# Optimization experiments

Measured on AMD Instinct MI355X. Metric: run time of the kernel, lower is better.

The kernel has to match this reference:

```python
import jax, jax.numpy as jnp
import numpy as np

B, C, H, W = 32, 256, 56, 56
NH, WS, SS = 8, 7, 3
N = WS * WS
EPS = 1e-5


def _rel_pos_index(ws):
    ch, cw = np.meshgrid(np.arange(ws), np.arange(ws), indexing='ij')
    coords = np.stack([ch.reshape(-1), cw.reshape(-1)])  # (2, N)
    rel = coords[:, :, None] - coords[:, None, :]        # (2, N, N)
    rel = rel.transpose(1, 2, 0)
    rel[:, :, 0] += ws - 1
    rel[:, :, 1] += ws - 1
    rel[:, :, 0] *= 2 * ws - 1
    return rel.sum(-1)  # (N, N) int


def _attn_mask(Hh, Ww, ws, ss):
    img = np.zeros((Hh, Ww), dtype=np.float32)
    cnt = 0
    for hs in (slice(0, -ws), slice(-ws, -ss), slice(-ss, None)):
        for wsl in (slice(0, -ws), slice(-ws, -ss), slice(-ss, None)):
            img[hs, wsl] = cnt
            cnt += 1
    mw = img.reshape(Hh // ws, ws, Ww // ws, ws).transpose(0, 2, 1, 3).reshape(-1, ws * ws)
    am = mw[:, None, :] - mw[:, :, None]
    return np.where(am != 0, np.float32(-100.0), np.float32(0.0))  # (nW, N, N)

RPI = _rel_pos_index(WS)
AMASK = _attn_mask(H, W, WS, SS)


def _ln(x, w, b):
    mu = x.mean(-1, keepdims=True)
    var = ((x - mu) ** 2).mean(-1, keepdims=True)
    return (x - mu) * jax.lax.rsqrt(var + EPS) * w + b


def setup_inputs() -> dict:
    key = jax.random.key(0)
    ks = jax.random.split(key, 10)
    s = 0.02
    return {
        'x': jax.random.normal(ks[0], (B, C, H, W), jnp.float32),
        'qkv_w': jax.random.normal(ks[1], (3 * C, C), jnp.float32) * s,
        'q_bias': jnp.zeros((C,), jnp.float32),
        'v_bias': jnp.zeros((C,), jnp.float32),
        'proj_w': jax.random.normal(ks[2], (C, C), jnp.float32) * s,
        'proj_b': jnp.zeros((C,), jnp.float32),
        'rpb_table': jax.random.normal(ks[3], ((2 * WS - 1) * (2 * WS - 1), NH), jnp.float32) * s,
        'norm1_w': jnp.ones((C,), jnp.float32),
        'norm1_b': jnp.zeros((C,), jnp.float32),
        'norm2_w': jnp.ones((C,), jnp.float32),
        'norm2_b': jnp.zeros((C,), jnp.float32),
        'fc1_w': jax.random.normal(ks[4], (4 * C, C), jnp.float32) * s,
        'fc1_b': jnp.zeros((4 * C,), jnp.float32),
        'fc2_w': jax.random.normal(ks[5], (C, 4 * C), jnp.float32) * s,
        'fc2_b': jnp.zeros((C,), jnp.float32),
    }


def reference(x, qkv_w, q_bias, v_bias, proj_w, proj_b, rpb_table,
              norm1_w, norm1_b, norm2_w, norm2_b, fc1_w, fc1_b, fc2_w, fc2_b):
    b = x.shape[0]
    hd = C // NH
    scale = hd ** -0.5
    nWh, nWw = H // WS, W // WS
    nW = nWh * nWw

    # (B,C,H,W) -> (B, L, C)
    xs = x.transpose(0, 2, 3, 1).reshape(b, H * W, C)
    shortcut = xs
    xn = _ln(xs, norm1_w, norm1_b).reshape(b, H, W, C)
    # cyclic shift
    xn = jnp.roll(xn, (-SS, -SS), axis=(1, 2))
    # window partition -> (B*nW, N, C)
    xw = xn.reshape(b, nWh, WS, nWw, WS, C).transpose(0, 1, 3, 2, 4, 5).reshape(b * nW, N, C)

    qkv_bias = jnp.concatenate([q_bias, jnp.zeros_like(v_bias), v_bias])
    qkv = xw @ qkv_w.T + qkv_bias                      # (B_, N, 3C)
    qkv = qkv.reshape(b * nW, N, 3, NH, hd).transpose(2, 0, 3, 1, 4)
    q, k, v = qkv[0], qkv[1], qkv[2]                   # (B_, NH, N, hd)

    attn = jnp.einsum('whnd,whmd->whnm', q * scale, k)  # (B_, NH, N, N)
    bias = rpb_table[RPI.reshape(-1)].reshape(N, N, NH).transpose(2, 0, 1)
    attn = attn + bias[None]
    attn = attn.reshape(b, nW, NH, N, N) + jnp.asarray(AMASK)[None, :, None]
    attn = jax.nn.softmax(attn.reshape(b * nW, NH, N, N), axis=-1)

    out = jnp.einsum('whnm,whmd->whnd', attn, v)        # (B_, NH, N, hd)
    out = out.transpose(0, 2, 1, 3).reshape(b * nW, N, C)
    out = out @ proj_w.T + proj_b

    # window reverse + un-shift
    out = out.reshape(b, nWh, nWw, WS, WS, C).transpose(0, 1, 3, 2, 4, 5).reshape(b, H, W, C)
    out = jnp.roll(out, (SS, SS), axis=(1, 2)).reshape(b, H * W, C)

    xs = shortcut + out
    h = _ln(xs, norm2_w, norm2_b)
    h = jax.nn.relu(h @ fc1_w.T + fc1_b) @ fc2_w.T + fc2_b
    xs = xs + h
    return xs.reshape(b, H, W, C).transpose(0, 3, 1, 2)
```

## Files before the change

kernel.cpp:

```cpp
#include <hip/hip_runtime.h>
#include <math.h>

#define EPS 1e-5f

constexpr int Bc = 32, Cc = 256, Hc = 56, Wc = 56;
constexpr int NHc = 8, HDc = 32, WSc = 7, SSc = 3;
constexpr int NTOK = 49;
constexpr int NWIN = 64;
constexpr int Lc = Hc * Wc;
constexpr int Mrows = Bc * NWIN * NTOK;
constexpr int GIMG = 8;
constexpr int NGRP = Bc / GIMG;
constexpr int ROWS_G = GIMG * Lc;
constexpr int WIN_G = GIMG * NWIN;

typedef short bf16x8 __attribute__((ext_vector_type(8)));
typedef float f32x4 __attribute__((ext_vector_type(4)));
typedef unsigned short u16x8 __attribute__((ext_vector_type(8)));

__device__ __forceinline__ float bf2f(unsigned short u) {
    return __uint_as_float(((unsigned)u) << 16);
}
__device__ __forceinline__ unsigned short f2bf(float f) {
    unsigned x = __float_as_uint(f);
    return (unsigned short)((x + 0x7fffu + ((x >> 16) & 1u)) >> 16);
}

__global__ __launch_bounds__(256) void k_prep(const float* __restrict__ qkv_w,
                                              const float* __restrict__ proj_w,
                                              const float* __restrict__ w1,
                                              const float* __restrict__ w2,
                                              const float* __restrict__ qb,
                                              const float* __restrict__ vb,
                                              unsigned short* __restrict__ qkv_wb,
                                              unsigned short* __restrict__ proj_wb,
                                              unsigned short* __restrict__ w1t,
                                              unsigned short* __restrict__ w2t,
                                              float* __restrict__ qkvb) {
    int i = blockIdx.x * 256 + threadIdx.x;
    if (i < 768) qkvb[i] = (i < 256) ? qb[i] : ((i < 512) ? 0.f : vb[i - 512]);
    if (i < 196608) qkv_wb[i] = f2bf(qkv_w[i]);
    if (i < 65536)  proj_wb[i] = f2bf(proj_w[i]);
    if (i < 262144) {
        int n1 = i >> 8, k1 = i & 255;
        w1t[((n1 >> 4) * 32 + (k1 >> 3)) * 128 + (n1 & 15) * 8 + (k1 & 7)] = f2bf(w1[i]);
        int n2 = i >> 10, k2 = i & 1023;
        w2t[((k2 >> 6) * 32 + (n2 >> 4) * 2 + ((k2 >> 5) & 1)) * 512 +
            ((k2 >> 3) & 3) * 128 + (n2 & 15) * 8 + (k2 & 7)] = f2bf(w2[i]);
    }
}

__global__ __launch_bounds__(256) void k_ln1_part(const float* __restrict__ x,
                                                  const float* __restrict__ n1w,
                                                  const float* __restrict__ n1b,
                                                  unsigned short* __restrict__ xw,
                                                  unsigned short* __restrict__ xres,
                                                  int b0) {
    __shared__ float s[Cc * 57];
    __shared__ float mu[Wc], rs[Wc];
    int bg = blockIdx.x / Hc, h = blockIdx.x % Hc;
    int b = b0 + bg;
    int t = threadIdx.x;
    const float* xp = x + ((size_t)b * Cc) * Lc + h * Wc;
    for (int idx = t; idx < Cc * Wc; idx += 256) {
        int c = idx / Wc, w = idx % Wc;
        s[c * 57 + w] = xp[(size_t)c * Lc + w];
    }
    __syncthreads();
    int lane = t & 63, wv = t >> 6;
    for (int p = wv; p < Wc; p += 4) {
        float sum = 0.f, sq = 0.f;
        #pragma unroll
        for (int k = 0; k < 4; ++k) {
            float v = s[(lane + 64 * k) * 57 + p];
            sum += v; sq += v * v;
        }
        #pragma unroll
        for (int off = 32; off; off >>= 1) {
            sum += __shfl_xor(sum, off);
            sq  += __shfl_xor(sq, off);
        }
        if (lane == 0) {
            float m = sum / Cc;
            mu[p] = m;
            rs[p] = rsqrtf(sq / Cc - m * m + EPS);
        }
    }
    __syncthreads();
    float wc_ = n1w[t], bc_ = n1b[t];
    int hr = (h + Hc - SSc) % Hc;
    int whh = hr / WSc, th = hr % WSc;
    for (int p = 0; p < Wc; ++p) {
        float raw = s[t * 57 + p];
        xres[((size_t)bg * Lc + h * Wc + p) * Cc + t] = f2bf(raw);
        int wr = (p + Wc - SSc) % Wc;
        int www = wr / WSc, tw = wr % WSc;
        int row = (b * NWIN + whh * 8 + www) * NTOK + th * WSc + tw;
        float v = (raw - mu[p]) * rs[p] * wc_ + bc_;
        xw[(size_t)row * Cc + t] = f2bf(v);
    }
}

__global__ __launch_bounds__(256) void k_gemm_mfma(const unsigned short* __restrict__ A,
                                                   const unsigned short* __restrict__ W,
                                                   const float* __restrict__ bias,
                                                   unsigned short* __restrict__ outb,
                                                   int K, int Nd) {
    __shared__ unsigned short As[128 * 32];
    __shared__ unsigned short Bs[128 * 32];
    int t = threadIdx.x;
    int l = t & 63, w = t >> 6;
    int wm = w & 1, wn = w >> 1;
    int m0 = blockIdx.x * 128, n0 = blockIdx.y * 128;
    int lr = l & 15, lg = l >> 4;

    f32x4 acc[4][4];
    #pragma unroll
    for (int i = 0; i < 4; ++i)
        #pragma unroll
        for (int j = 0; j < 4; ++j)
            acc[i][j] = (f32x4){0.f, 0.f, 0.f, 0.f};

    for (int kt = 0; kt < K; kt += 32) {
        #pragma unroll
        for (int s = 0; s < 2; ++s) {
            int cid = t + s * 256;
            int row = cid >> 2, ch = cid & 3;
            u16x8 va = *(const u16x8*)(A + (size_t)(m0 + row) * K + kt + ch * 8);
            u16x8 vb = *(const u16x8*)(W + (size_t)(n0 + row) * K + kt + ch * 8);
            int off = (row * 32 + ch * 8) ^ ((row & 7) << 3);
            *(u16x8*)&As[off] = va;
            *(u16x8*)&Bs[off] = vb;
        }
        __syncthreads();
        bf16x8 af[4], bfr[4];
        #pragma unroll
        for (int i = 0; i < 4; ++i) {
            int ra = wm * 64 + i * 16 + lr;
            af[i] = *(bf16x8*)&As[(ra * 32 + lg * 8) ^ ((ra & 7) << 3)];
            int rb = wn * 64 + i * 16 + lr;
            bfr[i] = *(bf16x8*)&Bs[(rb * 32 + lg * 8) ^ ((rb & 7) << 3)];
        }
        #pragma unroll
        for (int i = 0; i < 4; ++i)
            #pragma unroll
            for (int j = 0; j < 4; ++j)
                acc[i][j] = __builtin_amdgcn_mfma_f32_16x16x32_bf16(af[i], bfr[j], acc[i][j], 0, 0, 0);
        __syncthreads();
    }

    float bj[4];
    #pragma unroll
    for (int j = 0; j < 4; ++j) bj[j] = bias[n0 + wn * 64 + j * 16 + lr];
    #pragma unroll
    for (int i = 0; i < 4; ++i)
        #pragma unroll
        for (int j = 0; j < 4; ++j) {
            int col = n0 + wn * 64 + j * 16 + lr;
            #pragma unroll
            for (int r = 0; r < 4; ++r) {
                int row = m0 + wm * 64 + i * 16 + lg * 4 + r;
                outb[(size_t)row * Nd + col] = f2bf(acc[i][j][r] + bj[j]);
            }
        }
}

__global__ __launch_bounds__(256) void k_gemm_proj(const unsigned short* __restrict__ A,
                                                   const unsigned short* __restrict__ W,
                                                   const float* __restrict__ bias,
                                                   const unsigned short* __restrict__ xres,
                                                   unsigned short* __restrict__ xs) {
    __shared__ unsigned short As[128 * 32];
    __shared__ unsigned short Bs[128 * 32];
    constexpr int K = 256;
    int t = threadIdx.x;
    int l = t & 63, w = t >> 6;
    int wm = w & 1, wn = w >> 1;
    int m0 = blockIdx.x * 128, n0 = blockIdx.y * 128;
    int lr = l & 15, lg = l >> 4;

    f32x4 acc[4][4];
    #pragma unroll
    for (int i = 0; i < 4; ++i)
        #pragma unroll
        for (int j = 0; j < 4; ++j)
            acc[i][j] = (f32x4){0.f, 0.f, 0.f, 0.f};

    for (int kt = 0; kt < K; kt += 32) {
        #pragma unroll
        for (int s = 0; s < 2; ++s) {
            int cid = t + s * 256;
            int row = cid >> 2, ch = cid & 3;
            u16x8 va = *(const u16x8*)(A + (size_t)(m0 + row) * K + kt + ch * 8);
            u16x8 vb = *(const u16x8*)(W + (size_t)(n0 + row) * K + kt + ch * 8);
            int off = (row * 32 + ch * 8) ^ ((row & 7) << 3);
            *(u16x8*)&As[off] = va;
            *(u16x8*)&Bs[off] = vb;
        }
        __syncthreads();
        bf16x8 af[4], bfr[4];
        #pragma unroll
        for (int i = 0; i < 4; ++i) {
            int ra = wm * 64 + i * 16 + lr;
            af[i] = *(bf16x8*)&As[(ra * 32 + lg * 8) ^ ((ra & 7) << 3)];
            int rb = wn * 64 + i * 16 + lr;
            bfr[i] = *(bf16x8*)&Bs[(rb * 32 + lg * 8) ^ ((rb & 7) << 3)];
        }
        #pragma unroll
        for (int i = 0; i < 4; ++i)
            #pragma unroll
            for (int j = 0; j < 4; ++j)
                acc[i][j] = __builtin_amdgcn_mfma_f32_16x16x32_bf16(af[i], bfr[j], acc[i][j], 0, 0, 0);
        __syncthreads();
    }

    float bj[4];
    #pragma unroll
    for (int j = 0; j < 4; ++j) bj[j] = bias[n0 + wn * 64 + j * 16 + lr];
    #pragma unroll
    for (int i = 0; i < 4; ++i)
        #pragma unroll
        for (int j = 0; j < 4; ++j) {
            int col = n0 + wn * 64 + j * 16 + lr;
            #pragma unroll
            for (int r = 0; r < 4; ++r) {
                int row = m0 + wm * 64 + i * 16 + lg * 4 + r;
                int wl = row / NTOK, tok = row - wl * NTOK;
                int bg = wl >> 6, wi = wl & 63;
                int hr = (wi >> 3) * 7 + tok / 7;
                int wr = (wi & 7) * 7 + tok % 7;
                int hh = hr + SSc; if (hh >= Hc) hh -= Hc;
                int ww = wr + SSc; if (ww >= Wc) ww -= Wc;
                size_t didx = ((size_t)bg * Lc + hh * Wc + ww) * Cc + col;
                float res = bf2f(xres[didx]);
                xs[didx] = f2bf(res + acc[i][j][r] + bj[j]);
            }
        }
}

__global__ __launch_bounds__(256) void k_attn(const unsigned short* __restrict__ qkv,
                                              const float* __restrict__ rpb,
                                              unsigned short* __restrict__ outb) {
    __shared__ unsigned short lds[4 * 6144 + 1352];
    unsigned short* rpbs = &lds[4 * 6144];
    int t = threadIdx.x;
    int w = t >> 6, l = t & 63;
    int lr = l & 15, lg = l >> 4;
    unsigned short* wl = &lds[w * 6144];
    unsigned short* Qs = wl;
    unsigned short* Ks = wl + 2048;
    unsigned short* Pm = wl;
    unsigned short* Vt = wl + 4096;

    for (int i = t; i < 1352; i += 256) rpbs[i] = f2bf(rpb[i]);

    int gid = blockIdx.x * 4 + w;
    int b_ = gid >> 3, hh = gid & 7;
    const unsigned short* base = qkv + (size_t)b_ * NTOK * 768 + hh * HDc;

    {
        int j = l;
        u16x8 vq[4], vk[4], vv[4];
        if (j < NTOK) {
            const unsigned short* rp = base + j * 768;
            #pragma unroll
            for (int s = 0; s < 4; ++s) {
                vq[s] = *(const u16x8*)(rp + s * 8);
                vk[s] = *(const u16x8*)(rp + 256 + s * 8);
                vv[s] = *(const u16x8*)(rp + 512 + s * 8);
            }
        } else {
            u16x8 z = {0, 0, 0, 0, 0, 0, 0, 0};
            #pragma unroll
            for (int s = 0; s < 4; ++s) { vq[s] = z; vk[s] = z; vv[s] = z; }
        }
        #pragma unroll
        for (int s = 0; s < 4; ++s) {
            int off = (j * 32 + s * 8) ^ ((j & 7) << 3);
            *(u16x8*)&Qs[off] = vq[s];
            *(u16x8*)&Ks[off] = vk[s];
        }
        #pragma unroll
        for (int s = 0; s < 4; ++s)
            #pragma unroll
            for (int e = 0; e < 8; ++e) {
                int d = s * 8 + e;
                Vt[d * 64 + (j ^ ((d & 7) << 3))] = ((unsigned short*)&vv[s])[e];
            }
    }
    __syncthreads();

    bf16x8 aq[4], bk[4];
    #pragma unroll
    for (int mt = 0; mt < 4; ++mt) {
        int row = mt * 16 + lr;
        int off = (row * 32 + lg * 8) ^ ((row & 7) << 3);
        aq[mt] = *(bf16x8*)&Qs[off];
        bk[mt] = *(bf16x8*)&Ks[off];
    }
    f32x4 sc[4][4];
    #pragma unroll
    for (int mt = 0; mt < 4; ++mt)
        #pragma unroll
        for (int nt = 0; nt < 4; ++nt)
            sc[mt][nt] = __builtin_amdgcn_mfma_f32_16x16x32_bf16(
                aq[mt], bk[nt], (f32x4){0.f, 0.f, 0.f, 0.f}, 0, 0, 0);

    const float scale = 0.17677669529663687f;
    int wi = b_ & 63, wh = wi >> 3, wwc = wi & 7;
    int jh[4], jw[4], ridJ[4];
    #pragma unroll
    for (int nt = 0; nt < 4; ++nt) {
        int j = nt * 16 + lr;
        jh[nt] = j / 7; jw[nt] = j - jh[nt] * 7;
        int gh = wh * 7 + jh[nt], gw = wwc * 7 + jw[nt];
        int rh = gh < 49 ? 0 : (gh < 53 ? 1 : 2);
        int rw = gw < 49 ? 0 : (gw < 53 ? 1 : 2);
        ridJ[nt] = rh * 3 + rw;
    }

    float rowrcp[4][4];
    #pragma unroll
    for (int mt = 0; mt < 4; ++mt) {
        #pragma unroll
        for (int r = 0; r < 4; ++r) {
            int i = mt * 16 + lg * 4 + r;
            int ih = i / 7, iw = i - ih * 7;
            int gh = wh * 7 + ih, gw = wwc * 7 + iw;
            int rhI = gh < 49 ? 0 : (gh < 53 ? 1 : 2);
            int rwI = gw < 49 ? 0 : (gw < 53 ? 1 : 2);
            int ridI = rhI * 3 + rwI;
            bool ivalid = (i < NTOK);
            float vals[4];
            float vmax = -1e30f;
            #pragma unroll
            for (int nt = 0; nt < 4; ++nt) {
                int j = nt * 16 + lr;
                float v = -1e30f;
                if (ivalid && j < NTOK) {
                    int rpi = (ih - jh[nt] + 6) * 13 + (iw - jw[nt] + 6);
                    float bv = bf2f(rpbs[rpi * 8 + hh]);
                    float msk = (ridI == ridJ[nt]) ? 0.f : -100.f;
                    v = sc[mt][nt][r] * scale + bv + msk;
                }
                vals[nt] = v;
                vmax = fmaxf(vmax, v);
            }
            #pragma unroll
            for (int off = 1; off < 16; off <<= 1)
                vmax = fmaxf(vmax, __shfl_xor(vmax, off));
            float s = 0.f;
            unsigned short pb[4];
            #pragma unroll
            for (int nt = 0; nt < 4; ++nt) {
                float e = (vals[nt] > -1e29f) ? __expf(vals[nt] - vmax) : 0.f;
                s += e;
                pb[nt] = f2bf(e);
            }
            #pragma unroll
            for (int off = 1; off < 16; off <<= 1)
                s += __shfl_xor(s, off);
            rowrcp[mt][r] = 1.f / s;
            #pragma unroll
            for (int nt = 0; nt < 4; ++nt) {
                int j = nt * 16 + lr;
                Pm[(i * 64 + j) ^ ((i & 7) << 3)] = pb[nt];
            }
        }
    }

    f32x4 o[4][2];
    #pragma unroll
    for (int mt = 0; mt < 4; ++mt)
        #pragma unroll
        for (int nt = 0; nt < 2; ++nt)
            o[mt][nt] = (f32x4){0.f, 0.f, 0.f, 0.f};
    #pragma unroll
    for (int ks = 0; ks < 2; ++ks) {
        bf16x8 ap[4], bv2[2];
        #pragma unroll
        for (int mt = 0; mt < 4; ++mt) {
            int row = mt * 16 + lr;
            ap[mt] = *(bf16x8*)&Pm[(row * 64 + ks * 32 + lg * 8) ^ ((row & 7) << 3)];
        }
        #pragma unroll
        for (int nt = 0; nt < 2; ++nt) {
            int n = nt * 16 + lr;
            bv2[nt] = *(bf16x8*)&Vt[(n * 64 + ks * 32 + lg * 8) ^ ((n & 7) << 3)];
        }
        #pragma unroll
        for (int mt = 0; mt < 4; ++mt)
            #pragma unroll
            for (int nt = 0; nt < 2; ++nt)
                o[mt][nt] = __builtin_amdgcn_mfma_f32_16x16x32_bf16(ap[mt], bv2[nt], o[mt][nt], 0, 0, 0);
    }

    #pragma unroll
    for (int mt = 0; mt < 4; ++mt)
        #pragma unroll
        for (int r = 0; r < 4; ++r) {
            int i = mt * 16 + lg * 4 + r;
            if (i < NTOK) {
                float rc = rowrcp[mt][r];
                #pragma unroll
                for (int nt = 0; nt < 2; ++nt) {
                    int d = nt * 16 + lr;
                    outb[((size_t)b_ * NTOK + i) * Cc + hh * HDc + d] = f2bf(o[mt][nt][r] * rc);
                }
            }
        }
}

#define HIDX(m, c) (((m) * 64 + (c)) ^ (((m) & 7) << 3))
__global__ __launch_bounds__(512) void k_mlp_fused(const unsigned short* __restrict__ xs,
                                                   const float* __restrict__ n2w,
                                                   const float* __restrict__ n2b,
                                                   const unsigned short* __restrict__ w1t,
                                                   const float* __restrict__ b1,
                                                   const unsigned short* __restrict__ w2t,
                                                   const float* __restrict__ b2,
                                                   float* __restrict__ out) {
    __shared__ unsigned short w1s[16384];
    __shared__ unsigned short w2s[16384];
    __shared__ unsigned short hid[8192];
    int t = threadIdx.x;
    int l = t & 63, w = t >> 6;
    int wm = w >> 1, wn = w & 1;
    int lr = l & 15, lg = l >> 4;
    int m0 = blockIdx.x * 128;

    bf16x8 xf[2][8];
    {
        #pragma unroll
        for (int mf = 0; mf < 2; ++mf) {
            int row = m0 + wm * 32 + mf * 16 + lr;
            const unsigned short* xrow = xs + (size_t)row * Cc;
            u16x8 raw[8];
            float sum = 0.f, sq = 0.f;
            #pragma unroll
            for (int ks = 0; ks < 8; ++ks) {
                raw[ks] = *(const u16x8*)(xrow + ks * 32 + lg * 8);
                #pragma unroll
                for (int e = 0; e < 8; ++e) {
                    float f = bf2f(raw[ks][e]);
                    sum += f; sq += f * f;
                }
            }
            sum += __shfl_xor(sum, 16); sq += __shfl_xor(sq, 16);
            sum += __shfl_xor(sum, 32); sq += __shfl_xor(sq, 32);
            float mu = sum / Cc;
            float rsg = rsqrtf(sq / Cc - mu * mu + EPS);
            #pragma unroll
            for (int ks = 0; ks < 8; ++ks) {
                #pragma unroll
                for (int e = 0; e < 8; ++e) {
                    int c = ks * 32 + lg * 8 + e;
                    float nv = (bf2f(raw[ks][e]) - mu) * rsg * n2w[c] + n2b[c];
                    ((unsigned short*)&xf[mf][ks])[e] = f2bf(nv);
                }
            }
        }
    }

    f32x4 acc2[2][8];
    #pragma unroll
    for (int mf = 0; mf < 2; ++mf)
        #pragma unroll
        for (int nf = 0; nf < 8; ++nf)
            acc2[mf][nf] = (f32x4){0.f, 0.f, 0.f, 0.f};

    u16x8 p1[4], p2[4];
    #pragma unroll
    for (int i = 0; i < 4; ++i) {
        int idx = (i * 512 + t) * 8;
        p1[i] = *(const u16x8*)(w1t + idx);
        p2[i] = *(const u16x8*)(w2t + idx);
    }

    for (int ch = 0; ch < 16; ++ch) {
        #pragma unroll
        for (int i = 0; i < 4; ++i) {
            int idx = (i * 512 + t) * 8;
            *(u16x8*)&w1s[idx] = p1[i];
            *(u16x8*)&w2s[idx] = p2[i];
        }
        __syncthreads();
        if (ch < 15) {
            const unsigned short* n1 = w1t + (ch + 1) * 16384;
            const unsigned short* n2 = w2t + (ch + 1) * 16384;
            #pragma unroll
            for (int i = 0; i < 4; ++i) {
                int idx = (i * 512 + t) * 8;
                p1[i] = *(const u16x8*)(n1 + idx);
                p2[i] = *(const u16x8*)(n2 + idx);
            }
        }
        {
            f32x4 acc1[2][2];
            #pragma unroll
            for (int mf = 0; mf < 2; ++mf)
                #pragma unroll
                for (int nf = 0; nf < 2; ++nf)
                    acc1[mf][nf] = (f32x4){0.f, 0.f, 0.f, 0.f};
            #pragma unroll
            for (int ks = 0; ks < 8; ++ks) {
                #pragma unroll
                for (int nf = 0; nf < 2; ++nf) {
                    int ntl = wn * 2 + nf;
                    bf16x8 bfr = *(const bf16x8*)&w1s[ntl * 4096 + ks * 512 + l * 8];
                    acc1[0][nf] = __builtin_amdgcn_mfma_f32_16x16x32_bf16(xf[0][ks], bfr, acc1[0][nf], 0, 0, 0);
                    acc1[1][nf] = __builtin_amdgcn_mfma_f32_16x16x32_bf16(xf[1][ks], bfr, acc1[1][nf], 0, 0, 0);
                }
            }
            #pragma unroll
            for (int nf = 0; nf < 2; ++nf) {
                float b1n = b1[ch * 64 + wn * 32 + nf * 16 + lr];
                #pragma unroll
                for (int mf = 0; mf < 2; ++mf)
                    #pragma unroll
                    for (int r = 0; r < 4; ++r) {
                        int m = wm * 32 + mf * 16 + lg * 4 + r;
                        hid[HIDX(m, wn * 32 + nf * 16 + lr)] =
                            f2bf(fmaxf(acc1[mf][nf][r] + b1n, 0.f));
                    }
            }
        }
        __syncthreads();
        {
            bf16x8 a[2][2];
            #pragma unroll
            for (int mf = 0; mf < 2; ++mf)
                #pragma unroll
                for (int ks = 0; ks < 2; ++ks) {
                    int m = wm * 32 + mf * 16 + lr;
                    a[mf][ks] = *(const bf16x8*)&hid[HIDX(m, ks * 32 + lg * 8)];
                }
            #pragma unroll
            for (int ks = 0; ks < 2; ++ks)
                #pragma unroll
                for (int nf = 0; nf < 8; ++nf) {
                    int nt = (wn * 128 + nf * 16) >> 4;
                    bf16x8 bfr = *(const bf16x8*)&w2s[(nt * 2 + ks) * 512 + l * 8];
                    acc2[0][nf] = __builtin_amdgcn_mfma_f32_16x16x32_bf16(a[0][ks], bfr, acc2[0][nf], 0, 0, 0);
                    acc2[1][nf] = __builtin_amdgcn_mfma_f32_16x16x32_bf16(a[1][ks], bfr, acc2[1][nf], 0, 0, 0);
                }
        }
        __syncthreads();
    }

    int b0i = m0 / Lc, l0 = m0 % Lc;
    #pragma unroll
    for (int nf = 0; nf < 8; ++nf) {
        int c = wn * 128 + nf * 16 + lr;
        float b2c = b2[c];
        #pragma unroll
        for (int mf = 0; mf < 2; ++mf)
            #pragma unroll
            for (int r = 0; r < 4; ++r) {
                int m = wm * 32 + mf * 16 + lg * 4 + r;
                float res = bf2f(xs[(size_t)(m0 + m) * Cc + c]);
                int lm = l0 + m;
                int bi = b0i + (lm >= Lc);
                if (lm >= Lc) lm -= Lc;
                out[((size_t)bi * Cc + c) * Lc + lm] = acc2[mf][nf][r] + b2c + res;
            }
    }
}

extern "C" void kernel_launch(void* const* d_in, const int* in_sizes, int n_in,
                              void* d_out, int out_size, void* d_ws, size_t ws_size,
                              hipStream_t stream) {
    const float* x      = (const float*)d_in[0];
    const float* qkv_w  = (const float*)d_in[1];
    const float* q_bias = (const float*)d_in[2];
    const float* v_bias = (const float*)d_in[3];
    const float* proj_w = (const float*)d_in[4];
    const float* proj_b = (const float*)d_in[5];
    const float* rpb    = (const float*)d_in[6];
    const float* n1w    = (const float*)d_in[7];
    const float* n1b    = (const float*)d_in[8];
    const float* n2w    = (const float*)d_in[9];
    const float* n2b    = (const float*)d_in[10];
    const float* w1     = (const float*)d_in[11];
    const float* b1     = (const float*)d_in[12];
    const float* w2     = (const float*)d_in[13];
    const float* b2     = (const float*)d_in[14];

    char* ws = (char*)d_ws;
    const size_t SZ_BF16 = (size_t)Mrows * Cc * 2;
    unsigned short* xw      = (unsigned short*)ws;
    float*          qkvb    = (float*)(ws + SZ_BF16);
    unsigned short* qkv_wb  = (unsigned short*)(ws + SZ_BF16 + 3072);
    unsigned short* proj_wb = qkv_wb + 196608;
    unsigned short* w1t     = proj_wb + 65536;
    unsigned short* w2t     = w1t + 262144;

    unsigned short* qkv_s  = (unsigned short*)d_out;
    unsigned short* attn_s = qkv_s + (size_t)ROWS_G * 768;
    unsigned short* xres_s = attn_s + (size_t)ROWS_G * Cc;

    k_prep<<<1024, 256, 0, stream>>>(qkv_w, proj_w, w1, w2, q_bias, v_bias,
                                     qkv_wb, proj_wb, w1t, w2t, qkvb);

    for (int g = 0; g < NGRP; ++g) {
        unsigned short* xw_g = xw + (size_t)g * ROWS_G * Cc;
        k_ln1_part<<<GIMG * Hc, 256, 0, stream>>>(x, n1w, n1b, xw, xres_s, g * GIMG);
        k_gemm_mfma<<<dim3(ROWS_G / 128, 768 / 128), 256, 0, stream>>>(
            xw_g, qkv_wb, qkvb, qkv_s, 256, 768);
        k_attn<<<WIN_G * NHc / 4, 256, 0, stream>>>(qkv_s, rpb, attn_s);
        k_gemm_proj<<<dim3(ROWS_G / 128, 2), 256, 0, stream>>>(
            attn_s, proj_wb, proj_b, xres_s, xw_g);
    }

    k_mlp_fused<<<Mrows / 128, 512, 0, stream>>>(xw, n2w, n2b, w1t, b1, w2t, b2,
                                                 (float*)d_out);
}
```

Measured before the change: 609.8 us.

## Use direct global-to-LDS loads in GEMMs and transposed MFMA for MLP hidden stores

The two tiled GEMM kernels now stage A/W tiles with global_load_lds, which writes straight into shared memory and skips the register round trip. Each lane's source address is computed with an inverse swizzle so the LDS layout keeps the existing XOR swizzle. In the fused MLP, the first GEMM swaps its operands so each lane holds four consecutive hidden columns, allowing packed 4-wide bf16 stores into the swizzled hidden buffer instead of scalar stores. The risks are correctness of the inverse-swizzle mapping and the hidden-buffer index, which is written inline rather than through HIDX, and that the loop stays unpipelined, so load latency may still be exposed.

```diff
diff --git a/kernel.cpp b/kernel.cpp
--- a/kernel.cpp
+++ b/kernel.cpp
@@ -17,6 +17,7 @@
 typedef short bf16x8 __attribute__((ext_vector_type(8)));
 typedef float f32x4 __attribute__((ext_vector_type(4)));
 typedef unsigned short u16x8 __attribute__((ext_vector_type(8)));
+typedef unsigned short u16x4 __attribute__((ext_vector_type(4)));
 
 __device__ __forceinline__ float bf2f(unsigned short u) {
     return __uint_as_float(((unsigned)u) << 16);
@@ -24,6 +25,18 @@
 __device__ __forceinline__ unsigned short f2bf(float f) {
     unsigned x = __float_as_uint(f);
     return (unsigned short)((x + 0x7fffu + ((x >> 16) & 1u)) >> 16);
+}
+__device__ __forceinline__ void gload_lds16(const void* g, void* l) {
+    __builtin_amdgcn_global_load_lds(
+        (const __attribute__((address_space(1))) unsigned int*)g,
+        (__attribute__((address_space(3))) unsigned int*)l, 16, 0, 0);
+}
+__device__ __forceinline__ void inv_swz(int bp, int& row, int& ch) {
+    int b2 = ((bp >> 2) ^ (bp >> 4)) & 1;
+    int b1_ = ((bp >> 1) ^ (bp >> 3)) & 1;
+    int b0 = (bp ^ (bp >> 2) ^ (bp >> 4)) & 1;
+    int B = (bp & ~7) | (b2 << 2) | (b1_ << 1) | b0;
+    row = B >> 2; ch = B & 3;
 }
 
 __global__ __launch_bounds__(256) void k_prep(const float* __restrict__ qkv_w,
@@ -114,6 +127,18 @@
     int m0 = blockIdx.x * 128, n0 = blockIdx.y * 128;
     int lr = l & 15, lg = l >> 4;
 
+    int row0, ch0, row1, ch1;
+    inv_swz(w * 128 + l, row0, ch0);
+    inv_swz(w * 128 + 64 + l, row1, ch1);
+    const unsigned short* gA0 = A + (size_t)(m0 + row0) * K + ch0 * 8;
+    const unsigned short* gA1 = A + (size_t)(m0 + row1) * K + ch1 * 8;
+    const unsigned short* gB0 = W + (size_t)(n0 + row0) * K + ch0 * 8;
+    const unsigned short* gB1 = W + (size_t)(n0 + row1) * K + ch1 * 8;
+    unsigned short* lA0 = &As[(w * 128) * 8];
+    unsigned short* lA1 = &As[(w * 128 + 64) * 8];
+    unsigned short* lB0 = &Bs[(w * 128) * 8];
+    unsigned short* lB1 = &Bs[(w * 128 + 64) * 8];
+
     f32x4 acc[4][4];
     #pragma unroll
     for (int i = 0; i < 4; ++i)
@@ -122,16 +147,10 @@
             acc[i][j] = (f32x4){0.f, 0.f, 0.f, 0.f};
 
     for (int kt = 0; kt < K; kt += 32) {
-        #pragma unroll
-        for (int s = 0; s < 2; ++s) {
-            int cid = t + s * 256;
-            int row = cid >> 2, ch = cid & 3;
-            u16x8 va = *(const u16x8*)(A + (size_t)(m0 + row) * K + kt + ch * 8);
-            u16x8 vb = *(const u16x8*)(W + (size_t)(n0 + row) * K + kt + ch * 8);
-            int off = (row * 32 + ch * 8) ^ ((row & 7) << 3);
-            *(u16x8*)&As[off] = va;
-            *(u16x8*)&Bs[off] = vb;
-        }
+        gload_lds16(gA0 + kt, lA0);
+        gload_lds16(gA1 + kt, lA1);
+        gload_lds16(gB0 + kt, lB0);
+        gload_lds16(gB1 + kt, lB1);
         __syncthreads();
         bf16x8 af[4], bfr[4];
         #pragma unroll
@@ -179,6 +198,18 @@
     int m0 = blockIdx.x * 128, n0 = blockIdx.y * 128;
     int lr = l & 15, lg = l >> 4;
 
+    int row0, ch0, row1, ch1;
+    inv_swz(w * 128 + l, row0, ch0);
+    inv_swz(w * 128 + 64 + l, row1, ch1);
+    const unsigned short* gA0 = A + (size_t)(m0 + row0) * K + ch0 * 8;
+    const unsigned short* gA1 = A + (size_t)(m0 + row1) * K + ch1 * 8;
+    const unsigned short* gB0 = W + (size_t)(n0 + row0) * K + ch0 * 8;
+    const unsigned short* gB1 = W + (size_t)(n0 + row1) * K + ch1 * 8;
+    unsigned short* lA0 = &As[(w * 128) * 8];
+    unsigned short* lA1 = &As[(w * 128 + 64) * 8];
+    unsigned short* lB0 = &Bs[(w * 128) * 8];
+    unsigned short* lB1 = &Bs[(w * 128 + 64) * 8];
+
     f32x4 acc[4][4];
     #pragma unroll
     for (int i = 0; i < 4; ++i)
@@ -187,16 +218,10 @@
             acc[i][j] = (f32x4){0.f, 0.f, 0.f, 0.f};
 
     for (int kt = 0; kt < K; kt += 32) {
-        #pragma unroll
-        for (int s = 0; s < 2; ++s) {
-            int cid = t + s * 256;
-            int row = cid >> 2, ch = cid & 3;
-            u16x8 va = *(const u16x8*)(A + (size_t)(m0 + row) * K + kt + ch * 8);
-            u16x8 vb = *(const u16x8*)(W + (size_t)(n0 + row) * K + kt + ch * 8);
-            int off = (row * 32 + ch * 8) ^ ((row & 7) << 3);
-            *(u16x8*)&As[off] = va;
-            *(u16x8*)&Bs[off] = vb;
-        }
+        gload_lds16(gA0 + kt, lA0);
+        gload_lds16(gA1 + kt, lA1);
+        gload_lds16(gB0 + kt, lB0);
+        gload_lds16(gB1 + kt, lB1);
         __syncthreads();
         bf16x8 af[4], bfr[4];
         #pragma unroll
@@ -498,31 +523,38 @@
         {
             f32x4 acc1[2][2];
             #pragma unroll
-            for (int mf = 0; mf < 2; ++mf)
-                #pragma unroll
-                for (int nf = 0; nf < 2; ++nf)
-                    acc1[mf][nf] = (f32x4){0.f, 0.f, 0.f, 0.f};
+            for (int ht = 0; ht < 2; ++ht)
+                #pragma unroll
+                for (int mf = 0; mf < 2; ++mf)
+                    acc1[ht][mf] = (f32x4){0.f, 0.f, 0.f, 0.f};
             #pragma unroll
             for (int ks = 0; ks < 8; ++ks) {
-                #pragma unroll
-                for (int nf = 0; nf < 2; ++nf) {
-                    int ntl = wn * 2 + nf;
-                    bf16x8 bfr = *(const bf16x8*)&w1s[ntl * 4096 + ks * 512 + l * 8];
-                    acc1[0][nf] = __builtin_amdgcn_mfma_f32_16x16x32_bf16(xf[0][ks], bfr, acc1[0][nf], 0, 0, 0);
-                    acc1[1][nf] = __builtin_amdgcn_mfma_f32_16x16x32_bf16(xf[1][ks], bfr, acc1[1][nf], 0, 0, 0);
-                }
-            }
-            #pragma unroll
-            for (int nf = 0; nf < 2; ++nf) {
-                float b1n = b1[ch * 64 + wn * 32 + nf * 16 + lr];
-                #pragma unroll
-                for (int mf = 0; mf < 2; ++mf)
+                bf16x8 wfr[2];
+                #pragma unroll
+                for (int ht = 0; ht < 2; ++ht)
+                    wfr[ht] = *(const bf16x8*)&w1s[(wn * 2 + ht) * 4096 + ks * 512 + l * 8];
+                #pragma unroll
+                for (int ht = 0; ht < 2; ++ht) {
+                    acc1[ht][0] = __builtin_amdgcn_mfma_f32_16x16x32_bf16(wfr[ht], xf[0][ks], acc1[ht][0], 0, 0, 0);
+                    acc1[ht][1] = __builtin_amdgcn_mfma_f32_16x16x32_bf16(wfr[ht], xf[1][ks], acc1[ht][1], 0, 0, 0);
+                }
+            }
+            #pragma unroll
+            for (int ht = 0; ht < 2; ++ht) {
+                float b1v[4];
+                #pragma unroll
+                for (int r = 0; r < 4; ++r)
+                    b1v[r] = b1[ch * 64 + (wn * 2 + ht) * 16 + lg * 4 + r];
+                #pragma unroll
+                for (int mf = 0; mf < 2; ++mf) {
+                    u16x4 pk;
                     #pragma unroll
-                    for (int r = 0; r < 4; ++r) {
-                        int m = wm * 32 + mf * 16 + lg * 4 + r;
-                        hid[HIDX(m, wn * 32 + nf * 16 + lr)] =
-                            f2bf(fmaxf(acc1[mf][nf][r] + b1n, 0.f));
-                    }
+                    for (int r = 0; r < 4; ++r)
+                        pk[r] = f2bf(fmaxf(acc1[ht][mf][r] + b1v[r], 0.f));
+                    int m = wm * 32 + mf * 16 + lr;
+                    int off = m * 64 + ((((wn * 2 + ht) * 16) + lg * 4) ^ ((m & 7) << 3));
+                    *(u16x4*)&hid[off] = pk;
+                }
             }
         }
         __syncthreads();
```

Result: faster. 567.2 us (-7.0%).
